# Kernel optimization log

Measured on AMD Instinct MI355X. Metric: run time of the kernel, lower is better.

## Reference

```python
import jax, jax.numpy as jnp
import numpy as np
from jax import lax

E = 192      # hidden size
NH = 6       # attention heads
L = 6        # mixer blocks (permutation length)
CO = 256     # merging output channels
KH, KW = 7, 11   # locality window
LOCAL = (False, False, True, True, True, True)
B, H, W = 64, 8, 64


def skew(x, pad_value):
    # shift every row one step right, turning columns into diagonals (torch skew)
    rest = x.shape[:-2]
    Hd, Wd = x.shape[-2], x.shape[-1]
    x = jnp.pad(x, [(0, 0)] * (x.ndim - 1) + [(0, Hd)], constant_values=pad_value)
    x = x.reshape(*rest, -1)[..., : Hd * (Hd + Wd - 1)]
    x = x.reshape(*rest, Hd, Hd + Wd - 1)
    end = (Hd + Wd - 1) - (Wd // 2) + (Wd % 2 - 1)
    return x[..., Wd // 2 : end]


def make_mask(h, w, kh, kw):
    # boolean [h*w, h*w]; True inside the local window (torch: True = NOT allowed)
    m = jnp.ones((h, w, kh, kw), dtype=bool)
    m = m.transpose(0, 2, 1, 3)        # [h, kh, w, kw]
    m = skew(m, 0)                     # [h, kh, w, w]
    m = m.transpose(2, 3, 0, 1)        # [w, w, h, kh]
    m = skew(m, 0)                     # [w, w, h, h]
    m = m.transpose(2, 0, 3, 1)        # [h, w, h, w]
    return m.reshape(h * w, h * w)


def layernorm(x, g, b, eps=1e-5):
    mu = jnp.mean(x, axis=-1, keepdims=True)
    var = jnp.mean((x - mu) ** 2, axis=-1, keepdims=True)
    return (x - mu) / jnp.sqrt(var + eps) * g + b


def mha(x, mask, wi, bi, wo, bo, nh):
    # torch nn.MultiheadAttention (batch_first, self-attn, inference)
    b, s, e = x.shape
    hd = e // nh
    qkv = x @ wi.T + bi                                   # [b, s, 3e]
    q, k, v = jnp.split(qkv, 3, axis=-1)
    to_heads = lambda t: t.reshape(b, s, nh, hd).transpose(0, 2, 1, 3)
    q, k, v = to_heads(q), to_heads(k), to_heads(v)
    scores = jnp.einsum('bhqd,bhkd->bhqk', q, k) / jnp.sqrt(jnp.asarray(hd, x.dtype))
    if mask is not None:
        scores = jnp.where(mask, -jnp.inf, scores)
    attn = jax.nn.softmax(scores, axis=-1)
    out = jnp.einsum('bhqk,bhkd->bhqd', attn, v)
    out = out.transpose(0, 2, 1, 3).reshape(b, s, e)
    return out @ wo.T + bo


def mixer_block(x, mask, wi, bi, wo, bo, g1, b1, g2, b2, wm1, bm1, wm2, bm2):
    x = layernorm(x, g1, b1)
    x = mha(x, mask, wi, bi, wo, bo, NH) + x
    x = layernorm(x, g2, b2)
    h = jax.nn.relu(x @ wm1.T + bm1)
    return h @ wm2.T + bm2 + x


def fvtr_stage(image, in_w, in_b, out_w, out_b, ln1_g, ln1_b, ln2_g, ln2_b,
               w1, b1, w2, b2, conv_w, conv_b, mln_g, mln_b):
    bsz, c, h, w = image.shape
    x = jnp.swapaxes(image, -1, -3).reshape(bsz, w * h, c)   # [B, W*H, C]
    mask = make_mask(h, w, KH, KW)
    for i, loc in enumerate(LOCAL):
        x = mixer_block(x, mask if loc else None,
                        in_w[i], in_b[i], out_w[i], out_b[i],
                        ln1_g[i], ln1_b[i], ln2_g[i], ln2_b[i],
                        w1[i], b1[i], w2[i], b2[i])
    x = jnp.swapaxes(x.reshape(bsz, w, h, c), -1, -3)        # [B, C, H, W]
    # MergingBlock: conv (3,1) stride (2,1) pad (1,0) + channel LayerNorm
    y = lax.conv_general_dilated(x, conv_w, window_strides=(2, 1),
                                 padding=((1, 1), (0, 0)),
                                 dimension_numbers=('NCHW', 'OIHW', 'NCHW'))
    y = y + conv_b[None, :, None, None]
    y = jnp.moveaxis(y, 1, -1)
    y = layernorm(y, mln_g, mln_b)
    return jnp.moveaxis(y, -1, 1)


def setup_inputs() -> dict:
    key = jax.random.key(0)
    ks = jax.random.split(key, 8)
    s = 0.02
    return {
        'image': jax.random.normal(ks[0], (B, E, H, W), jnp.float32),
        'in_w':  s * jax.random.normal(ks[1], (L, 3 * E, E), jnp.float32),
        'in_b':  jnp.zeros((L, 3 * E), jnp.float32),
        'out_w': s * jax.random.normal(ks[2], (L, E, E), jnp.float32),
        'out_b': jnp.zeros((L, E), jnp.float32),
        'ln1_g': jnp.ones((L, E), jnp.float32),
        'ln1_b': jnp.zeros((L, E), jnp.float32),
        'ln2_g': jnp.ones((L, E), jnp.float32),
        'ln2_b': jnp.zeros((L, E), jnp.float32),
        'w1':    s * jax.random.normal(ks[3], (L, 4 * E, E), jnp.float32),
        'b1':    jnp.zeros((L, 4 * E), jnp.float32),
        'w2':    s * jax.random.normal(ks[4], (L, E, 4 * E), jnp.float32),
        'b2':    jnp.zeros((L, E), jnp.float32),
        'conv_w': s * jax.random.normal(ks[5], (CO, E, 3, 1), jnp.float32),
        'conv_b': jnp.zeros((CO,), jnp.float32),
        'mln_g': jnp.ones((CO,), jnp.float32),
        'mln_b': jnp.zeros((CO,), jnp.float32),
    }


def reference(image, in_w, in_b, out_w, out_b, ln1_g, ln1_b, ln2_g, ln2_b,
              w1, b1, w2, b2, conv_w, conv_b, mln_g, mln_b):
    return fvtr_stage(image, in_w, in_b, out_w, out_b, ln1_g, ln1_b, ln2_g, ln2_b,
                      w1, b1, w2, b2, conv_w, conv_b, mln_g, mln_b)
```

## Files before the change

kernel.cpp:

```cpp
#include <hip/hip_runtime.h>
#include <hip/hip_bf16.h>
#include <math.h>

#define Bn   64
#define Ssz  512
#define Ed   192
#define NHd  6
#define HDd  32
#define Ld   6
#define COd  256
#define Himg 8
#define Wimg 64
#define Mrows (Bn*Ssz)

typedef unsigned int  uint;
typedef unsigned short ushort;
using short8 = __attribute__((ext_vector_type(8))) short;
using f32x4  = __attribute__((ext_vector_type(4))) float;

__device__ inline ushort f2b(float f) {
    uint u = __builtin_bit_cast(uint, f);
    u = (u + 0x7FFFu + ((u >> 16) & 1u)) >> 16;
    return (ushort)u;
}

__device__ __forceinline__ float fexp2(float x) {
#if __has_builtin(__builtin_amdgcn_exp2f)
    return __builtin_amdgcn_exp2f(x);
#else
    return exp2f(x);
#endif
}

__device__ __forceinline__ uint cvt_pk_bf16(float a, float b) {
    uint r;
    asm("v_cvt_pk_bf16_f32 %0, %1, %2" : "=v"(r) : "v"(a), "v"(b));
    return r;
}

__device__ __forceinline__ void gload16(const ushort* g, ushort* l, int lane) {
#if __has_builtin(__builtin_amdgcn_global_load_lds)
    __builtin_amdgcn_global_load_lds(
        (const __attribute__((address_space(1))) uint*)g,
        (__attribute__((address_space(3))) uint*)l, 16, 0, 0);
#else
    *(uint4*)(l + (size_t)lane * 8) = *(const uint4*)g;
#endif
}

__global__ __launch_bounds__(256) void reshape_in(const float* __restrict__ img,
                                                  float* __restrict__ X) {
    int t = blockIdx.x * 256 + threadIdx.x;
    int c = t % Ed;
    int s = (t / Ed) % Ssz;
    int b = t / (Ed * Ssz);
    int w = s >> 3, h = s & 7;
    X[t] = img[(((size_t)b * Ed + c) * Himg + h) * Wimg + w];
}

__global__ __launch_bounds__(256) void f2b_arr(const float* __restrict__ in,
                                               ushort* __restrict__ out, int n) {
    int t = blockIdx.x * 256 + threadIdx.x;
    if (t < n) out[t] = f2b(in[t]);
}

__global__ __launch_bounds__(256) void conv_w_to_bf16(const float* __restrict__ cw,
                                                      ushort* __restrict__ out) {
    int t = blockIdx.x * 256 + threadIdx.x;
    if (t >= COd * 576) return;
    int co = t / 576, rem = t % 576;
    int kh = rem / Ed, c = rem % Ed;
    out[t] = f2b(cw[((size_t)co * Ed + c) * 3 + kh]);
}

__global__ __launch_bounds__(256) void ln_kernel(const float* __restrict__ in,
                                                 float* __restrict__ out,
                                                 ushort* __restrict__ outb,
                                                 const float* __restrict__ g,
                                                 const float* __restrict__ bb) {
    int row  = blockIdx.x * 4 + (threadIdx.x >> 6);
    int lane = threadIdx.x & 63;
    bool act = lane < 48;
    float4 v = make_float4(0.f, 0.f, 0.f, 0.f);
    if (act) v = ((const float4*)(in + (size_t)row * Ed))[lane];
    float s = v.x + v.y + v.z + v.w;
    #pragma unroll
    for (int off = 32; off > 0; off >>= 1) s += __shfl_xor(s, off);
    float mu = s * (1.f / 192.f);
    float4 d = make_float4(v.x - mu, v.y - mu, v.z - mu, v.w - mu);
    float qv = act ? (d.x*d.x + d.y*d.y + d.z*d.z + d.w*d.w) : 0.f;
    #pragma unroll
    for (int off = 32; off > 0; off >>= 1) qv += __shfl_xor(qv, off);
    float rstd = rsqrtf(qv * (1.f / 192.f) + 1e-5f);
    if (act) {
        float4 gg  = ((const float4*)g)[lane];
        float4 bbv = ((const float4*)bb)[lane];
        float4 y = make_float4(d.x * rstd * gg.x + bbv.x,
                               d.y * rstd * gg.y + bbv.y,
                               d.z * rstd * gg.z + bbv.z,
                               d.w * rstd * gg.w + bbv.w);
        ((float4*)(out + (size_t)row * Ed))[lane] = y;
        ushort4 yb;
        yb.x = f2b(y.x); yb.y = f2b(y.y); yb.z = f2b(y.z); yb.w = f2b(y.w);
        *(ushort4*)(outb + (size_t)row * Ed + lane * 4) = yb;
    }
}

template<int RELU, int RESID, int OBF, int VOUT>
__global__ __launch_bounds__(256) void gemm_mfma(
    const ushort* __restrict__ A, const ushort* __restrict__ Wt,
    const float* __restrict__ bias, const float* __restrict__ resid,
    float* __restrict__ C, ushort* __restrict__ Cb,
    ushort* __restrict__ qpout, ushort* __restrict__ kpout,
    ushort* __restrict__ vtout,
    int M, int N, int K)
{
    __shared__ __align__(16) ushort As[12288];
    __shared__ __align__(16) ushort Bs[6144];
    const int tid  = threadIdx.x;
    const int lane = tid & 63;
    const int wave = tid >> 6;
    const int wr = wave >> 1, wc = wave & 1;
    const int bm = blockIdx.x * 128;
    const int bn = blockIdx.y * 64;

    const ushort* Ag[6]; ushort* Al[6];
    #pragma unroll
    for (int i = 0; i < 6; ++i) {
        int fa = 4 * i + wave;
        int msub = fa / 3, ksub = fa % 3;
        int m = msub * 16 + (lane & 15);
        int k = ksub * 32 + ((lane >> 4) << 3);
        Ag[i] = A + (size_t)(bm + m) * K + k;
        Al[i] = As + fa * 512;
    }
    const ushort* Bg[3]; ushort* Bl[3];
    #pragma unroll
    for (int i = 0; i < 3; ++i) {
        int fb = 4 * i + wave;
        int nsub = fb / 3, ksub = fb % 3;
        int n = nsub * 16 + (lane & 15);
        int k = ksub * 32 + ((lane >> 4) << 3);
        Bg[i] = Wt + (size_t)(bn + n) * K + k;
        Bl[i] = Bs + fb * 512;
    }

    f32x4 acc[4][2];
    #pragma unroll
    for (int i = 0; i < 4; ++i)
        #pragma unroll
        for (int j = 0; j < 2; ++j) acc[i][j] = (f32x4){0.f, 0.f, 0.f, 0.f};

    for (int k0 = 0; k0 < K; k0 += 96) {
        #pragma unroll
        for (int i = 0; i < 6; ++i) gload16(Ag[i] + k0, Al[i], lane);
        #pragma unroll
        for (int i = 0; i < 3; ++i) gload16(Bg[i] + k0, Bl[i], lane);
        __syncthreads();
        #pragma unroll
        for (int ksub = 0; ksub < 3; ++ksub) {
            short8 af[4], bf[2];
            #pragma unroll
            for (int ms = 0; ms < 4; ++ms)
                af[ms] = *(const short8*)(As + (((wr*4+ms)*3 + ksub) * 64 + lane) * 8);
            #pragma unroll
            for (int ns = 0; ns < 2; ++ns)
                bf[ns] = *(const short8*)(Bs + (((wc*2+ns)*3 + ksub) * 64 + lane) * 8);
            #pragma unroll
            for (int ms = 0; ms < 4; ++ms)
                #pragma unroll
                for (int ns = 0; ns < 2; ++ns)
                    acc[ms][ns] = __builtin_amdgcn_mfma_f32_16x16x32_bf16(
                        af[ms], bf[ns], acc[ms][ns], 0, 0, 0);
        }
        __syncthreads();
    }

    int q = lane >> 4, colL = lane & 15;
    #pragma unroll
    for (int ms = 0; ms < 4; ++ms) {
        #pragma unroll
        for (int ns = 0; ns < 2; ++ns) {
            int row0 = bm + (wr*4 + ms) * 16 + q * 4;
            int col  = bn + (wc*2 + ns) * 16 + colL;
            float bvv = bias[col];
            float v[4];
            #pragma unroll
            for (int r = 0; r < 4; ++r) {
                v[r] = acc[ms][ns][r] + bvv;
                if (RELU) v[r] = fmaxf(v[r], 0.f);
                if (RESID) v[r] += resid[(size_t)(row0 + r) * N + col];
            }
            if (VOUT) {
                int bidx = row0 >> 9, srow = row0 & 511;
                if (col >= 384) {
                    int hh = (col - 384) >> 5, dd = (col - 384) & 31;
                    int sr = srow ^ ((((srow >> 2) ^ (srow >> 3)) & 1) * 12);
                    ushort4 pv;
                    pv.x = f2b(v[0]); pv.y = f2b(v[1]); pv.z = f2b(v[2]); pv.w = f2b(v[3]);
                    *(ushort4*)(vtout + (((size_t)(bidx * NHd + hh) * 32 + dd) << 9) + sr) = pv;
                } else {
                    ushort* dst = (col < 192) ? qpout : kpout;
                    int cc = (col < 192) ? col : col - 192;
                    if (col < 192) {
                        const float c2 = 0.2550547270628364f;
                        #pragma unroll
                        for (int r = 0; r < 4; ++r) v[r] *= c2;
                    }
                    int hh = cc >> 5, dd = cc & 31;
                    ushort* p = dst + ((size_t)(bidx * NHd + hh) << 14) + (size_t)srow * 32 + dd;
                    p[0]  = f2b(v[0]); p[32] = f2b(v[1]);
                    p[64] = f2b(v[2]); p[96] = f2b(v[3]);
                }
            } else {
                #pragma unroll
                for (int r = 0; r < 4; ++r) {
                    if (OBF) Cb[(size_t)(row0 + r) * N + col] = f2b(v[r]);
                    else     C [(size_t)(row0 + r) * N + col] = v[r];
                }
            }
        }
    }
}

template<int KIT, int LNOUT>
__global__ __launch_bounds__(256) void gemm_ln(
    const ushort* __restrict__ A, const ushort* __restrict__ Wt,
    const float* __restrict__ bias, const float* __restrict__ resid,
    const float* __restrict__ lng, const float* __restrict__ lnb,
    float* __restrict__ outf, ushort* __restrict__ outb)
{
    __shared__ __align__(16) ushort As[4096];
    __shared__ __align__(16) ushort Bs[12288];
    const int K = KIT * 64;
    const int lane = threadIdx.x & 63;
    const int wave = threadIdx.x >> 6;
    const int g = lane >> 4, ql = lane & 15;
    const int bm = blockIdx.x * 64;

    const ushort* Gp[8]; ushort* Lp[8];
    #pragma unroll
    for (int i = 0; i < 8; ++i) {
        int f = 4 * i + wave;
        if (f < 8) {
            int msub = f >> 1, ksub = f & 1;
            Gp[i] = A + (size_t)(bm + msub * 16 + ql) * K + ksub * 32 + g * 8;
            Lp[i] = As + f * 512;
        } else {
            int fb = f - 8, nsub = fb >> 1, ksub = fb & 1;
            Gp[i] = Wt + (size_t)(nsub * 16 + ql) * K + ksub * 32 + g * 8;
            Lp[i] = Bs + fb * 512;
        }
    }

    f32x4 acc[12];
    #pragma unroll
    for (int i = 0; i < 12; ++i) acc[i] = (f32x4){0.f, 0.f, 0.f, 0.f};

    for (int kc = 0; kc < KIT; ++kc) {
        #pragma unroll
        for (int i = 0; i < 8; ++i) gload16(Gp[i] + kc * 64, Lp[i], lane);
        __syncthreads();
        #pragma unroll
        for (int ksub = 0; ksub < 2; ++ksub) {
            short8 af = *(const short8*)(As + ((wave * 2 + ksub) * 64 + lane) * 8);
            #pragma unroll
            for (int ns = 0; ns < 12; ++ns) {
                short8 bf = *(const short8*)(Bs + ((ns * 2 + ksub) * 64 + lane) * 8);
                acc[ns] = __builtin_amdgcn_mfma_f32_16x16x32_bf16(af, bf, acc[ns], 0, 0, 0);
            }
        }
        __syncthreads();
    }

    float bi[12], gg[12], bb[12];
    #pragma unroll
    for (int ns = 0; ns < 12; ++ns) {
        int col = ns * 16 + ql;
        bi[ns] = bias[col];
        if (LNOUT) { gg[ns] = lng[col]; bb[ns] = lnb[col]; }
    }
    #pragma unroll
    for (int r = 0; r < 4; ++r) {
        int row = bm + wave * 16 + g * 4 + r;
        float v[12];
        #pragma unroll
        for (int ns = 0; ns < 12; ++ns)
            v[ns] = acc[ns][r] + bi[ns] + resid[(size_t)row * Ed + ns * 16 + ql];
        if (LNOUT) {
            float s = 0.f;
            #pragma unroll
            for (int ns = 0; ns < 12; ++ns) s += v[ns];
            s += __shfl_xor(s, 1); s += __shfl_xor(s, 2);
            s += __shfl_xor(s, 4); s += __shfl_xor(s, 8);
            float mu = s * (1.f / 192.f);
            float qv = 0.f;
            #pragma unroll
            for (int ns = 0; ns < 12; ++ns) { float d = v[ns] - mu; qv += d * d; }
            qv += __shfl_xor(qv, 1); qv += __shfl_xor(qv, 2);
            qv += __shfl_xor(qv, 4); qv += __shfl_xor(qv, 8);
            float rstd = rsqrtf(qv * (1.f / 192.f) + 1e-5f);
            #pragma unroll
            for (int ns = 0; ns < 12; ++ns) {
                float y = (v[ns] - mu) * rstd * gg[ns] + bb[ns];
                int col = ns * 16 + ql;
                outf[(size_t)row * Ed + col] = y;
                outb[(size_t)row * Ed + col] = f2b(y);
            }
        } else {
            #pragma unroll
            for (int ns = 0; ns < 12; ++ns)
                outf[(size_t)row * Ed + ns * 16 + ql] = v[ns];
        }
    }
}

template<int USE_MASK>
__global__ __launch_bounds__(256) void attn_mfma(const ushort* __restrict__ qp,
                                                 const ushort* __restrict__ kp,
                                                 const ushort* __restrict__ vt,
                                                 ushort* __restrict__ att) {
    const int bh = blockIdx.x;
    const int b = bh / NHd, h = bh % NHd;
    const int wave = threadIdx.x >> 6, lane = threadIdx.x & 63;
    const int g = lane >> 4, ql = lane & 15;
    const int qb = blockIdx.y * 128 + wave * 32;

    const ushort* qbase = qp + ((size_t)bh << 14);
    const ushort* kbase = kp + ((size_t)bh << 14);
    const ushort* vbase = vt + ((size_t)bh << 14);
    short8 qf[2];
    #pragma unroll
    for (int t = 0; t < 2; ++t)
        qf[t] = *(const short8*)(qbase + (size_t)(qb + t * 16 + ql) * 32 + g * 8);

    short8 onesf;
    #pragma unroll
    for (int j = 0; j < 8; ++j) onesf[j] = (short)0x3F80;

    uint m0[2], m1[2]; int qh[2];
    if (USE_MASK) {
        #pragma unroll
        for (int t = 0; t < 2; ++t) {
            int qwt = ((qb + t * 16) & 63) + ql;
            qh[t] = (qb + t * 16) >> 6;
            uint a0 = 0, a1 = 0;
            #pragma unroll
            for (int i = 0; i < 8; ++i) {
                int keyl = (i >> 2) * 16 + 4 * g + (i & 3);
                int d0 = keyl - qwt;      d0 = d0 < 0 ? -d0 : d0;
                int d1 = keyl + 32 - qwt; d1 = d1 < 0 ? -d1 : d1;
                if (d0 <= 5) a0 |= (1u << i);
                if (d1 <= 5) a1 |= (1u << i);
            }
            m0[t] = a0; m1[t] = a1;
        }
    }

    f32x4 o0[2], o1[2], o2[2];
    #pragma unroll
    for (int t = 0; t < 2; ++t) {
        o0[t] = (f32x4){0.f,0.f,0.f,0.f};
        o1[t] = (f32x4){0.f,0.f,0.f,0.f};
        o2[t] = (f32x4){0.f,0.f,0.f,0.f};
    }
    const f32x4 z = {0.f,0.f,0.f,0.f};

    short8 kA0, kA1, kB0, kB1, vA0, vA1, vB0, vB1;
    short8 pa[2];

    auto LKA = [&](int kt) {
        kA0 = *(const short8*)(kbase + (size_t)(kt * 32 + ql) * 32 + g * 8);
        kA1 = *(const short8*)(kbase + (size_t)(kt * 32 + 16 + ql) * 32 + g * 8);
    };
    auto LKB = [&](int kt) {
        kB0 = *(const short8*)(kbase + (size_t)(kt * 32 + ql) * 32 + g * 8);
        kB1 = *(const short8*)(kbase + (size_t)(kt * 32 + 16 + ql) * 32 + g * 8);
    };
    auto LVA = [&](int kt) {
        vA0 = *(const short8*)(vbase + (size_t)ql * 512 + kt * 32 + 8 * g);
        vA1 = *(const short8*)(vbase + (size_t)(16 + ql) * 512 + kt * 32 + 8 * g);
    };
    auto LVB = [&](int kt) {
        vB0 = *(const short8*)(vbase + (size_t)ql * 512 + kt * 32 + 8 * g);
        vB1 = *(const short8*)(vbase + (size_t)(16 + ql) * 512 + kt * 32 + 8 * g);
    };

    auto QK = [&](int kt, short8 k0, short8 k1) {
        #pragma unroll
        for (int t = 0; t < 2; ++t) {
            f32x4 st0 = __builtin_amdgcn_mfma_f32_16x16x32_bf16(k0, qf[t], z, 0, 0, 0);
            f32x4 st1 = __builtin_amdgcn_mfma_f32_16x16x32_bf16(k1, qf[t], z, 0, 0, 0);
            float p8[8];
            #pragma unroll
            for (int r = 0; r < 4; ++r) {
                p8[r]     = fexp2(st0[r]);
                p8[4 + r] = fexp2(st1[r]);
            }
            if (USE_MASK) {
                int dh = (kt >> 1) - qh[t]; dh = dh < 0 ? -dh : dh;
                if (dh <= 3) {
                    uint mm = (kt & 1) ? m1[t] : m0[t];
                    #pragma unroll
                    for (int i = 0; i < 8; ++i)
                        if ((mm >> i) & 1u) p8[i] = 0.f;
                }
            }
            uint Au = cvt_pk_bf16(p8[0], p8[1]);
            uint Bu = cvt_pk_bf16(p8[2], p8[3]);
            uint Cu = cvt_pk_bf16(p8[4], p8[5]);
            uint Du = cvt_pk_bf16(p8[6], p8[7]);
            asm("v_permlane32_swap_b32 %0, %1" : "+v"(Au), "+v"(Cu));
            asm("v_permlane32_swap_b32 %0, %1" : "+v"(Bu), "+v"(Du));
            union { uint u[4]; short8 s; } pk;
            pk.u[0] = Au; pk.u[1] = Bu; pk.u[2] = Cu; pk.u[3] = Du;
            pa[t] = pk.s;
        }
    };
    auto PV = [&](short8 v0, short8 v1) {
        #pragma unroll
        for (int t = 0; t < 2; ++t) {
            o0[t] = __builtin_amdgcn_mfma_f32_16x16x32_bf16(pa[t], v0, o0[t], 0, 0, 0);
            o1[t] = __builtin_amdgcn_mfma_f32_16x16x32_bf16(pa[t], v1, o1[t], 0, 0, 0);
            o2[t] = __builtin_amdgcn_mfma_f32_16x16x32_bf16(pa[t], onesf, o2[t], 0, 0, 0);
        }
    };

    LKA(0); LVA(0); LKB(1); LVB(1);
    #pragma unroll
    for (int ii = 0; ii < 7; ++ii) {
        const int i = 2 * ii;
        QK(i, kA0, kA1);  PV(vA0, vA1);  LKA(i + 2); LVA(i + 2);
        QK(i + 1, kB0, kB1); PV(vB0, vB1); LKB(i + 3); LVB(i + 3);
    }
    QK(14, kA0, kA1); PV(vA0, vA1);
    QK(15, kB0, kB1); PV(vB0, vB1);

    ushort* op = att + (size_t)b * Ssz * Ed + h * 32;
    #pragma unroll
    for (int t = 0; t < 2; ++t) {
        #pragma unroll
        for (int r = 0; r < 4; ++r) {
            float iv = 1.f / o2[t][r];
            int row = qb + t * 16 + 4 * g + r;
            op[(size_t)row * Ed + ql]      = f2b(o0[t][r] * iv);
            op[(size_t)row * Ed + 16 + ql] = f2b(o1[t][r] * iv);
        }
    }
}

__global__ __launch_bounds__(256) void im2col(const float* __restrict__ X,
                                              ushort* __restrict__ A2) {
    int t = blockIdx.x * 256 + threadIdx.x;
    int col = t % 576;
    int r   = t / 576;
    int kh = col / Ed, c = col % Ed;
    int w = r & 63, ho = (r >> 6) & 3, b = r >> 8;
    int hin = 2 * ho + kh - 1;
    float v = 0.f;
    if (hin >= 0 && hin < Himg)
        v = X[((size_t)(b * Ssz + w * Himg + hin)) * Ed + c];
    A2[t] = f2b(v);
}

__global__ __launch_bounds__(256) void ln_out_kernel(const float* __restrict__ C2,
                                                     const float* __restrict__ g,
                                                     const float* __restrict__ beta,
                                                     float* __restrict__ out) {
    __shared__ float lds[32 * 257];
    int w0 = blockIdx.x * 32, ho = blockIdx.y, b = blockIdx.z;
    int tid = threadIdx.x;
    size_t rbase = ((size_t)b * 4 + ho) * 64 + w0;

    for (int i = 0; i < 32; ++i)
        lds[i * 257 + tid] = C2[(rbase + i) * COd + tid];
    __syncthreads();

    int wv = tid >> 6, lane = tid & 63;
    for (int rr = 0; rr < 8; ++rr) {
        int i = wv * 8 + rr;
        float v0 = lds[i*257 + lane], v1 = lds[i*257 + lane + 64];
        float v2 = lds[i*257 + lane + 128], v3 = lds[i*257 + lane + 192];
        float s = v0 + v1 + v2 + v3;
        #pragma unroll
        for (int off = 32; off > 0; off >>= 1) s += __shfl_xor(s, off);
        float mu = s * (1.f / 256.f);
        float d0 = v0-mu, d1 = v1-mu, d2 = v2-mu, d3 = v3-mu;
        float qv = d0*d0 + d1*d1 + d2*d2 + d3*d3;
        #pragma unroll
        for (int off = 32; off > 0; off >>= 1) qv += __shfl_xor(qv, off);
        float rstd = rsqrtf(qv * (1.f / 256.f) + 1e-5f);
        lds[i*257 + lane]       = d0 * rstd * g[lane]       + beta[lane];
        lds[i*257 + lane + 64]  = d1 * rstd * g[lane + 64]  + beta[lane + 64];
        lds[i*257 + lane + 128] = d2 * rstd * g[lane + 128] + beta[lane + 128];
        lds[i*257 + lane + 192] = d3 * rstd * g[lane + 192] + beta[lane + 192];
    }
    __syncthreads();

    int w = tid & 31, half = tid >> 5;
    for (int j = 0; j < 32; ++j) {
        int co = half + j * 8;
        out[(((size_t)b * COd + co) * 4 + ho) * Wimg + w0 + w] = lds[w * 257 + co];
    }
}

extern "C" void kernel_launch(void* const* d_in, const int* in_sizes, int n_in,
                              void* d_out, int out_size, void* d_ws, size_t ws_size,
                              hipStream_t stream) {
    const float* image = (const float*)d_in[0];
    const float* in_w  = (const float*)d_in[1];
    const float* in_b  = (const float*)d_in[2];
    const float* out_w = (const float*)d_in[3];
    const float* out_b = (const float*)d_in[4];
    const float* ln1_g = (const float*)d_in[5];
    const float* ln1_b = (const float*)d_in[6];
    const float* ln2_g = (const float*)d_in[7];
    const float* ln2_b = (const float*)d_in[8];
    const float* w1    = (const float*)d_in[9];
    const float* b1    = (const float*)d_in[10];
    const float* w2    = (const float*)d_in[11];
    const float* b2    = (const float*)d_in[12];
    const float* convw = (const float*)d_in[13];
    const float* convb = (const float*)d_in[14];
    const float* mln_g = (const float*)d_in[15];
    const float* mln_b = (const float*)d_in[16];
    float* out = (float*)d_out;
    float* ws  = (float*)d_ws;

    float* F1   = ws;
    float* F2   = ws + 6291456;
    float* BIG  = ws + 12582912;
    ushort* QP   = (ushort*)BIG;
    ushort* KP   = (ushort*)(BIG + 3145728);
    ushort* VT   = (ushort*)(BIG + 6291456);
    ushort* Hb   = (ushort*)BIG;
    ushort* A2b  = (ushort*)BIG;
    float*  C2   = BIG + 4718592;
    ushort* XNb  = (ushort*)(BIG + 12582912);
    ushort* ATTb = (ushort*)(ws + 28311552);
    ushort* Wb   = (ushort*)(ws + 31457280);

    ushort* in_wb  = Wb;
    ushort* out_wb = Wb + 663552;
    ushort* w1b    = Wb + 884736;
    ushort* w2b    = Wb + 1769472;
    ushort* cwb    = Wb + 2654208;

    reshape_in<<<Mrows * Ed / 256, 256, 0, stream>>>(image, F2);
    f2b_arr<<<(663552 + 255) / 256, 256, 0, stream>>>(in_w,  in_wb,  663552);
    f2b_arr<<<(221184 + 255) / 256, 256, 0, stream>>>(out_w, out_wb, 221184);
    f2b_arr<<<(884736 + 255) / 256, 256, 0, stream>>>(w1,    w1b,    884736);
    f2b_arr<<<(884736 + 255) / 256, 256, 0, stream>>>(w2,    w2b,    884736);
    conv_w_to_bf16<<<(147456 + 255) / 256, 256, 0, stream>>>(convw, cwb);

    ln_kernel<<<Mrows / 4, 256, 0, stream>>>(F2, F1, XNb, ln1_g, ln1_b);

    for (int i = 0; i < Ld; ++i) {
        gemm_mfma<0,0,1,1><<<dim3(Mrows/128, 9), 256, 0, stream>>>(
            XNb, in_wb + (size_t)i * 3*Ed*Ed, in_b + i * 3*Ed,
            nullptr, nullptr, nullptr, QP, KP, VT, Mrows, 3*Ed, Ed);
        if (i >= 2) attn_mfma<1><<<dim3(Bn * NHd, 4), 256, 0, stream>>>(QP, KP, VT, ATTb);
        else        attn_mfma<0><<<dim3(Bn * NHd, 4), 256, 0, stream>>>(QP, KP, VT, ATTb);
        gemm_ln<3,1><<<Mrows/64, 256, 0, stream>>>(
            ATTb, out_wb + (size_t)i * Ed*Ed, out_b + i*Ed,
            F1, ln2_g + i*Ed, ln2_b + i*Ed, F2, XNb);
        gemm_mfma<1,0,1,0><<<dim3(Mrows/128, 12), 256, 0, stream>>>(
            XNb, w1b + (size_t)i * 4*Ed*Ed, b1 + i * 4*Ed,
            nullptr, nullptr, Hb, nullptr, nullptr, nullptr, Mrows, 4*Ed, Ed);
        if (i < Ld - 1) {
            gemm_ln<12,1><<<Mrows/64, 256, 0, stream>>>(
                Hb, w2b + (size_t)i * 4*Ed*Ed, b2 + i*Ed,
                F2, ln1_g + (i+1)*Ed, ln1_b + (i+1)*Ed, F1, XNb);
        } else {
            gemm_ln<12,0><<<Mrows/64, 256, 0, stream>>>(
                Hb, w2b + (size_t)i * 4*Ed*Ed, b2 + i*Ed,
                F2, nullptr, nullptr, F1, nullptr);
        }
    }

    im2col<<<9437184 / 256, 256, 0, stream>>>(F1, A2b);
    gemm_mfma<0,0,0,0><<<dim3(16384/128, 4), 256, 0, stream>>>(
        A2b, cwb, convb, nullptr, C2, nullptr, nullptr, nullptr, nullptr,
        16384, COd, 576);
    ln_out_kernel<<<dim3(2, 4, Bn), 256, 0, stream>>>(C2, mln_g, mln_b, out);
}
```

Measured before the change: 1.095 ms.

## Software-pipeline QK^T scores one tile ahead of softmax and PV in attention

Restructures the attention inner loop so the QK^T MFMAs for the next key tile are issued before the exp/mask/pack work of the current tile. K tiles are triple-buffered and V tiles double-buffered to hide load latency. The PV MFMA block is also wrapped in raised wave priority via s_setprio. This overlaps MFMA latency with VALU exp work, at the cost of more live registers (extra score and K buffers), which could reduce occupancy or cause spills.

```diff
diff --git a/kernel.cpp b/kernel.cpp
--- a/kernel.cpp
+++ b/kernel.cpp
@@ -366,36 +366,33 @@
     }
     const f32x4 z = {0.f,0.f,0.f,0.f};
 
-    short8 kA0, kA1, kB0, kB1, vA0, vA1, vB0, vB1;
+    short8 kb_[3][2];
+    short8 vb_[2][2];
+    f32x4  st_[2][4];
     short8 pa[2];
 
-    auto LKA = [&](int kt) {
-        kA0 = *(const short8*)(kbase + (size_t)(kt * 32 + ql) * 32 + g * 8);
-        kA1 = *(const short8*)(kbase + (size_t)(kt * 32 + 16 + ql) * 32 + g * 8);
+    auto LK = [&](int kt, short8* d) {
+        d[0] = *(const short8*)(kbase + (size_t)(kt * 32 + ql) * 32 + g * 8);
+        d[1] = *(const short8*)(kbase + (size_t)(kt * 32 + 16 + ql) * 32 + g * 8);
     };
-    auto LKB = [&](int kt) {
-        kB0 = *(const short8*)(kbase + (size_t)(kt * 32 + ql) * 32 + g * 8);
-        kB1 = *(const short8*)(kbase + (size_t)(kt * 32 + 16 + ql) * 32 + g * 8);
+    auto LV = [&](int kt, short8* d) {
+        d[0] = *(const short8*)(vbase + (size_t)ql * 512 + kt * 32 + 8 * g);
+        d[1] = *(const short8*)(vbase + (size_t)(16 + ql) * 512 + kt * 32 + 8 * g);
     };
-    auto LVA = [&](int kt) {
-        vA0 = *(const short8*)(vbase + (size_t)ql * 512 + kt * 32 + 8 * g);
-        vA1 = *(const short8*)(vbase + (size_t)(16 + ql) * 512 + kt * 32 + 8 * g);
+    auto S = [&](const short8* k, f32x4* st) {
+        st[0] = __builtin_amdgcn_mfma_f32_16x16x32_bf16(k[0], qf[0], z, 0, 0, 0);
+        st[1] = __builtin_amdgcn_mfma_f32_16x16x32_bf16(k[1], qf[0], z, 0, 0, 0);
+        st[2] = __builtin_amdgcn_mfma_f32_16x16x32_bf16(k[0], qf[1], z, 0, 0, 0);
+        st[3] = __builtin_amdgcn_mfma_f32_16x16x32_bf16(k[1], qf[1], z, 0, 0, 0);
     };
-    auto LVB = [&](int kt) {
-        vB0 = *(const short8*)(vbase + (size_t)ql * 512 + kt * 32 + 8 * g);
-        vB1 = *(const short8*)(vbase + (size_t)(16 + ql) * 512 + kt * 32 + 8 * g);
-    };
-
-    auto QK = [&](int kt, short8 k0, short8 k1) {
+    auto F = [&](int kt, const f32x4* st) {
         #pragma unroll
         for (int t = 0; t < 2; ++t) {
-            f32x4 st0 = __builtin_amdgcn_mfma_f32_16x16x32_bf16(k0, qf[t], z, 0, 0, 0);
-            f32x4 st1 = __builtin_amdgcn_mfma_f32_16x16x32_bf16(k1, qf[t], z, 0, 0, 0);
             float p8[8];
             #pragma unroll
             for (int r = 0; r < 4; ++r) {
-                p8[r]     = fexp2(st0[r]);
-                p8[4 + r] = fexp2(st1[r]);
+                p8[r]     = fexp2(st[t*2][r]);
+                p8[4 + r] = fexp2(st[t*2+1][r]);
             }
             if (USE_MASK) {
                 int dh = (kt >> 1) - qh[t]; dh = dh < 0 ? -dh : dh;
@@ -417,24 +414,28 @@
             pa[t] = pk.s;
         }
     };
-    auto PV = [&](short8 v0, short8 v1) {
+    auto PV = [&](const short8* v) {
         #pragma unroll
         for (int t = 0; t < 2; ++t) {
-            o0[t] = __builtin_amdgcn_mfma_f32_16x16x32_bf16(pa[t], v0, o0[t], 0, 0, 0);
-            o1[t] = __builtin_amdgcn_mfma_f32_16x16x32_bf16(pa[t], v1, o1[t], 0, 0, 0);
+            o0[t] = __builtin_amdgcn_mfma_f32_16x16x32_bf16(pa[t], v[0], o0[t], 0, 0, 0);
+            o1[t] = __builtin_amdgcn_mfma_f32_16x16x32_bf16(pa[t], v[1], o1[t], 0, 0, 0);
             o2[t] = __builtin_amdgcn_mfma_f32_16x16x32_bf16(pa[t], onesf, o2[t], 0, 0, 0);
         }
     };
 
-    LKA(0); LVA(0); LKB(1); LVB(1);
-    #pragma unroll
-    for (int ii = 0; ii < 7; ++ii) {
-        const int i = 2 * ii;
-        QK(i, kA0, kA1);  PV(vA0, vA1);  LKA(i + 2); LVA(i + 2);
-        QK(i + 1, kB0, kB1); PV(vB0, vB1); LKB(i + 3); LVB(i + 3);
-    }
-    QK(14, kA0, kA1); PV(vA0, vA1);
-    QK(15, kB0, kB1); PV(vB0, vB1);
+    LK(0, kb_[0]); LK(1, kb_[1]); LK(2, kb_[2]);
+    LV(0, vb_[0]); LV(1, vb_[1]);
+    S(kb_[0], st_[0]);
+    #pragma unroll
+    for (int kt = 0; kt < 16; ++kt) {
+        if (kt < 15) S(kb_[(kt + 1) % 3], st_[(kt + 1) & 1]);
+        if (kt < 13) LK(kt + 3, kb_[kt % 3]);
+        F(kt, st_[kt & 1]);
+        __builtin_amdgcn_s_setprio(1);
+        PV(vb_[kt & 1]);
+        __builtin_amdgcn_s_setprio(0);
+        if (kt < 14) LV(kt + 2, vb_[kt & 1]);
+    }
 
     ushort* op = att + (size_t)b * Ssz * Ed + h * 32;
     #pragma unroll
```

Measured after the change: 1.081 ms. No clear change (-1.3%).
